# Optimization experiments

Hardware: AMD Instinct MI355X
Metric: run time of the kernel (lower is better)

## Reference

```python
import jax, jax.numpy as jnp
import numpy as np

B, L, D, N, R = 8, 64, 1024, 128, 64  # batch, seq(=channels), dim(=dim_inner), d_state, dt_rank


def setup_inputs() -> dict:
    key = jax.random.key(0)
    ks = jax.random.split(key, 8)
    sc = lambda k, sh, f: jax.random.normal(k, sh, jnp.float32) * f
    return {
        "x": sc(ks[0], (B, L, D), 1.0),
        "proj_w": sc(ks[1], (D, D), D ** -0.5),
        "proj_b": jnp.zeros((D,), jnp.float32),
        "conv_w": sc(ks[2], (L, L, 3), (L * 3) ** -0.5),  # (out_ch, in_ch, k)
        "conv_b": jnp.zeros((L,), jnp.float32),
        "dbc_w": sc(ks[3], (R + 2 * N, D), D ** -0.5),
        "dt_w": sc(ks[4], (D, R), R ** -0.5),
        "dt_b": sc(ks[5], (D,), 0.02),
        "A_log": jnp.log(jnp.broadcast_to(jnp.arange(1, N + 1, dtype=jnp.float32), (D, N))),
        "Dp": jnp.ones((D,), jnp.float32),
    }


def _ssm(x, dbc_w, dt_w, dt_b, A_log, Dp):
    # x: (B, L, ED) with ED == D
    A = -jnp.exp(A_log)                          # (ED, N)
    dbc = x @ dbc_w.T                            # (B, L, R + 2N)
    delta, Bm, Cm = jnp.split(dbc, [R, R + N], axis=-1)
    delta = jax.nn.softplus(delta @ dt_w.T + dt_b)            # (B, L, ED)
    dA = jnp.exp(delta[..., None] * A)                        # (B, L, ED, N)
    dBx = delta[..., None] * Bm[:, :, None, :] * x[..., None]  # (B, L, ED, N)

    def comb(c1, c2):
        a1, b1 = c1
        a2, b2 = c2
        return a1 * a2, a2 * b1 + b2

    _, hs = jax.lax.associative_scan(comb, (dA, dBx), axis=1)  # (B, L, ED, N)
    y = jnp.einsum("blen,bln->ble", hs, Cm)
    return y + Dp * x


def reference(x, proj_w, proj_b, conv_w, conv_b, dbc_w, dt_w, dt_b, A_log, Dp):
    skip = x
    xp = x @ proj_w.T + proj_b          # shared proj; x_one == x_two pre-activation
    x_two = jax.nn.silu(xp)
    # Conv1d treats seq axis (len L) as channels, convolving over the feature axis.
    x_one = jax.lax.conv_general_dilated(
        xp, conv_w, window_strides=(1,), padding=[(1, 1)],
        dimension_numbers=("NCH", "OIH", "NCH"),
    ) + conv_b[None, :, None]
    x_one = jax.nn.silu(x_one)
    x_one = _ssm(x_one, dbc_w, dt_w, dt_b, A_log, Dp)
    out = x_one * x_two + skip
    return out @ proj_w.T + proj_b
```

## Files before the change

kernel.cpp:

```cpp
#include <hip/hip_runtime.h>
#include <math.h>

#define B_ 8
#define L_ 64
#define D_ 1024
#define N_ 128
#define R_ 64

typedef unsigned short u16;
typedef __bf16 bf16x8 __attribute__((ext_vector_type(8)));
typedef u16 u16x8 __attribute__((ext_vector_type(8)));
typedef float floatx4 __attribute__((ext_vector_type(4)));

__device__ __forceinline__ float silu_f(float x) { return x / (1.f + __expf(-x)); }
__device__ __forceinline__ float softplus_f(float x) {
    return fmaxf(x, 0.f) + log1pf(__expf(-fabsf(x)));
}

__launch_bounds__(256)
__global__ void prep_bf16(const float* __restrict__ pw,
                          const float* __restrict__ dbcw,
                          const float* __restrict__ xin,
                          __bf16* __restrict__ pw_b,
                          __bf16* __restrict__ dbcw_b,
                          __bf16* __restrict__ x_b)
{
    int gid = blockIdx.x * 256 + threadIdx.x;
    const float* src; __bf16* dst; int off;
    if (gid < 131072)       { src = pw;   dst = pw_b;   off = gid * 8; }
    else if (gid < 172032)  { src = dbcw; dst = dbcw_b; off = (gid - 131072) * 8; }
    else if (gid < 237568)  { src = xin;  dst = x_b;    off = (gid - 172032) * 8; }
    else return;
    float4 f0 = *reinterpret_cast<const float4*>(src + off);
    float4 f1 = *reinterpret_cast<const float4*>(src + off + 4);
    bf16x8 v;
    v[0] = (__bf16)f0.x; v[1] = (__bf16)f0.y; v[2] = (__bf16)f0.z; v[3] = (__bf16)f0.w;
    v[4] = (__bf16)f1.x; v[5] = (__bf16)f1.y; v[6] = (__bf16)f1.z; v[7] = (__bf16)f1.w;
    *reinterpret_cast<bf16x8*>(dst + off) = v;
}

template <int ACT, int OUTF32>
__launch_bounds__(256)
__global__ void gemm_mfma(const u16* __restrict__ A, int lda,
                          const u16* __restrict__ W, int ldw,
                          const float* __restrict__ bias,
                          void* __restrict__ Cp, __bf16* __restrict__ C2,
                          int ldc, int K)
{
    __shared__ u16 As[32 * 64];
    __shared__ u16 Bs[64 * 64];
    const int tid = threadIdx.x;
    const int l   = tid & 63;
    const int w   = tid >> 6;
    const int wm  = w >> 1, wn = w & 1;
    const int m0  = blockIdx.y * 32;
    const int n0  = blockIdx.x * 64;

    const int ar = tid >> 3, ac = tid & 7;

    u16x8 sa, sb0, sb1;
    auto issue_loads = [&](int k0) {
        sa  = *reinterpret_cast<const u16x8*>(A + (size_t)(m0 + ar) * lda + k0 + ac * 8);
        sb0 = *reinterpret_cast<const u16x8*>(W + (size_t)(n0 + ar) * ldw + k0 + ac * 8);
        sb1 = *reinterpret_cast<const u16x8*>(W + (size_t)(n0 + 32 + ar) * ldw + k0 + ac * 8);
    };
    auto stage = [&]() {
        *reinterpret_cast<u16x8*>(&As[ar * 64 + ((ac ^ (ar & 7)) * 8)]) = sa;
        *reinterpret_cast<u16x8*>(&Bs[ar * 64 + ((ac ^ (ar & 7)) * 8)]) = sb0;
        const int r2 = 32 + ar;
        *reinterpret_cast<u16x8*>(&Bs[r2 * 64 + ((ac ^ (r2 & 7)) * 8)]) = sb1;
    };

    floatx4 acc[2] = {(floatx4)0.f, (floatx4)0.f};

    issue_loads(0);
    stage();
    __syncthreads();
    const int NT = K / 64;
    for (int t = 0; t < NT; ++t) {
        if (t + 1 < NT) issue_loads((t + 1) * 64);
        #pragma unroll
        for (int s = 0; s < 2; ++s) {
            const int ra = wm * 16 + (l & 15);
            const int ca = (s * 4 + (l >> 4)) ^ (ra & 7);
            bf16x8 a = *reinterpret_cast<const bf16x8*>(&As[ra * 64 + ca * 8]);
            #pragma unroll
            for (int nf = 0; nf < 2; ++nf) {
                const int rb = wn * 32 + nf * 16 + (l & 15);
                const int cb = (s * 4 + (l >> 4)) ^ (rb & 7);
                bf16x8 b = *reinterpret_cast<const bf16x8*>(&Bs[rb * 64 + cb * 8]);
                acc[nf] = __builtin_amdgcn_mfma_f32_16x16x32_bf16(a, b, acc[nf], 0, 0, 0);
            }
        }
        __syncthreads();
        if (t + 1 < NT) { stage(); __syncthreads(); }
    }

    #pragma unroll
    for (int nf = 0; nf < 2; ++nf) {
        const int n = n0 + wn * 32 + nf * 16 + (l & 15);
        const float bj = bias ? bias[n] : 0.f;
        #pragma unroll
        for (int r = 0; r < 4; ++r) {
            const int m = m0 + wm * 16 + (l >> 4) * 4 + r;
            float c = acc[nf][r] + bj;
            if (ACT == 2) c = softplus_f(c);
            const size_t idx = (size_t)m * ldc + n;
            if (OUTF32) ((float*)Cp)[idx] = c;
            else        ((__bf16*)Cp)[idx] = (__bf16)c;
            if (ACT == 1) C2[idx] = (__bf16)silu_f(c);
        }
    }
}

__launch_bounds__(256)
__global__ void conv_silu(const __bf16* __restrict__ xp,
                          const float* __restrict__ conv_w,
                          const float* __restrict__ conv_b,
                          __bf16* __restrict__ x_one)
{
    __shared__ float ws[192][65];
    __shared__ float xs[64][34];
    const int tid = threadIdx.x;
    const int b = blockIdx.y;
    const int d0 = blockIdx.x * 32;

    for (int idx = tid; idx < 64 * 64 * 3; idx += 256) {
        int lo = idx / 192, r = idx % 192;
        ws[r][lo] = conv_w[idx];
    }
    for (int idx = tid; idx < 64 * 34; idx += 256) {
        int li = idx / 34, dd = idx % 34;
        int g = d0 - 1 + dd;
        xs[li][dd] = (g >= 0 && g < D_) ? (float)xp[((size_t)b * L_ + li) * D_ + g] : 0.f;
    }
    __syncthreads();

    const int lo = tid >> 2;
    const int dbase = (tid & 3) * 8;
    float acc[8] = {};
    #pragma unroll 4
    for (int li = 0; li < 64; ++li) {
        float w0 = ws[li * 3 + 0][lo];
        float w1 = ws[li * 3 + 1][lo];
        float w2 = ws[li * 3 + 2][lo];
        float xv[10];
        #pragma unroll
        for (int j = 0; j < 10; ++j) xv[j] = xs[li][dbase + j];
        #pragma unroll
        for (int i = 0; i < 8; ++i)
            acc[i] = fmaf(w0, xv[i], fmaf(w1, xv[i + 1], fmaf(w2, xv[i + 2], acc[i])));
    }
    float bb = conv_b[lo];
    bf16x8 v;
    #pragma unroll
    for (int i = 0; i < 8; ++i) v[i] = (__bf16)silu_f(acc[i] + bb);
    *reinterpret_cast<bf16x8*>(&x_one[((size_t)b * L_ + lo) * D_ + d0 + dbase]) = v;
}

__launch_bounds__(256)
__global__ void ssm_scan(const __bf16* __restrict__ dbc,
                         const float* __restrict__ dt_w,
                         const float* __restrict__ dt_b,
                         const __bf16* __restrict__ xo_in,
                         const __bf16* __restrict__ xt_in,
                         const float* __restrict__ skip,
                         const float* __restrict__ A_log,
                         const float* __restrict__ Dp,
                         __bf16* __restrict__ out_mid)
{
    __shared__ u16 bcs[64][320];
    __shared__ float dtw_s[4][64];
    __shared__ float2 dlx[4][64];
    __shared__ float pt[4][16][65];
    const int tid = threadIdx.x;
    const int w = tid >> 6, ln = tid & 63;
    const int b = blockIdx.y;
    const int d = blockIdx.x * 4 + w;

    {
        const u16* src = (const u16*)dbc + (size_t)b * L_ * 320;
        #pragma unroll
        for (int i = tid; i < 2560; i += 256) {
            int lr = i / 40, c = i % 40;
            *reinterpret_cast<u16x8*>(&bcs[lr][c * 8]) =
                *reinterpret_cast<const u16x8*>(src + lr * 320 + c * 8);
        }
    }
    dtw_s[w][ln] = dt_w[(size_t)d * 64 + ln];
    const float xo_own = (float)xo_in[((size_t)b * L_ + ln) * D_ + d];
    const float a0 = -__expf(A_log[(size_t)d * N_ + ln]);
    const float a1 = -__expf(A_log[(size_t)d * N_ + 64 + ln]);
    const float dtb = dt_b[d];
    __syncthreads();

    float accd = dtb;
    #pragma unroll
    for (int k = 0; k < 64; ++k) {
        int kk = (k + ln) & 63;
        accd = fmaf((float)*reinterpret_cast<const __bf16*>(&bcs[ln][kk]),
                    dtw_s[w][kk], accd);
    }
    const float dl_own = softplus_f(accd);
    dlx[w][ln] = make_float2(dl_own, xo_own);
    __syncthreads();

    float h0 = 0.f, h1 = 0.f;
    float ych[4];
    const int rr = ln & 15, qq = ln >> 4;

    #pragma unroll
    for (int cch = 0; cch < 4; ++cch) {
        #pragma unroll
        for (int r = 0; r < 16; ++r) {
            const int l = cch * 16 + r;
            float2 dd = dlx[w][l];
            float dx = dd.x * dd.y;
            float B0 = (float)*reinterpret_cast<const __bf16*>(&bcs[l][64 + ln]);
            float B1 = (float)*reinterpret_cast<const __bf16*>(&bcs[l][128 + ln]);
            float C0 = (float)*reinterpret_cast<const __bf16*>(&bcs[l][192 + ln]);
            float C1 = (float)*reinterpret_cast<const __bf16*>(&bcs[l][256 + ln]);
            h0 = fmaf(__expf(dd.x * a0), h0, dx * B0);
            h1 = fmaf(__expf(dd.x * a1), h1, dx * B1);
            pt[w][r][ln] = fmaf(h0, C0, h1 * C1);
        }
        float sum = 0.f;
        #pragma unroll
        for (int j = 0; j < 4; ++j) {
            float4 v = *reinterpret_cast<const float4*>(&pt[w][rr][qq * 16 + j * 4]);
            sum += (v.x + v.y) + (v.z + v.w);
        }
        sum += __shfl_xor(sum, 16, 64);
        sum += __shfl_xor(sum, 32, 64);
        ych[cch] = sum;
    }

    float ysel = (qq == 0) ? ych[0] : (qq == 1) ? ych[1] : (qq == 2) ? ych[2] : ych[3];
    size_t idx = ((size_t)b * L_ + ln) * D_ + d;
    float y = ysel + Dp[d] * xo_own;
    out_mid[idx] = (__bf16)(y * (float)xt_in[idx] + skip[idx]);
}

extern "C" void kernel_launch(void* const* d_in, const int* in_sizes, int n_in,
                              void* d_out, int out_size, void* d_ws, size_t ws_size,
                              hipStream_t stream)
{
    const float* x      = (const float*)d_in[0];
    const float* proj_w = (const float*)d_in[1];
    const float* proj_b = (const float*)d_in[2];
    const float* conv_w = (const float*)d_in[3];
    const float* conv_b = (const float*)d_in[4];
    const float* dbc_w  = (const float*)d_in[5];
    const float* dt_w   = (const float*)d_in[6];
    const float* dt_b   = (const float*)d_in[7];
    const float* A_log  = (const float*)d_in[8];
    const float* Dp     = (const float*)d_in[9];
    float* out = (float*)d_out;

    __bf16* base    = (__bf16*)d_ws;
    __bf16* xp_b    = base;
    __bf16* xtwo_b  = xp_b + 524288;
    __bf16* xone_b  = xtwo_b + 524288;
    __bf16* dbc_b   = xone_b + 524288;
    __bf16* omid_b  = dbc_b + 163840;
    __bf16* pw_b    = omid_b + 524288;
    __bf16* dbcw_b  = pw_b + 1048576;
    __bf16* x_b     = dbcw_b + 327680;

    prep_bf16<<<928, 256, 0, stream>>>(proj_w, dbc_w, x, pw_b, dbcw_b, x_b);
    gemm_mfma<1, 0><<<dim3(16, 16), 256, 0, stream>>>(
        (const u16*)x_b, D_, (const u16*)pw_b, D_, proj_b, xp_b, xtwo_b, D_, D_);
    conv_silu<<<dim3(32, B_), 256, 0, stream>>>(xp_b, conv_w, conv_b, xone_b);
    gemm_mfma<0, 0><<<dim3(5, 16), 256, 0, stream>>>(
        (const u16*)xone_b, D_, (const u16*)dbcw_b, D_, nullptr, dbc_b, nullptr, 320, D_);
    ssm_scan<<<dim3(256, B_), 256, 0, stream>>>(
        dbc_b, dt_w, dt_b, xone_b, xtwo_b, x, A_log, Dp, omid_b);
    gemm_mfma<0, 1><<<dim3(16, 16), 256, 0, stream>>>(
        (const u16*)omid_b, D_, (const u16*)pw_b, D_, proj_b, out, nullptr, D_, D_);
}
```

Before: 163.1 us.

## Double-buffer GEMM smem, shrink tiles, transpose B/C output for vectorized scan reads

Result: faster. 156.7 us (-3.9%).

```diff
diff --git a/kernel.cpp b/kernel.cpp
--- a/kernel.cpp
+++ b/kernel.cpp
@@ -39,76 +39,101 @@
     *reinterpret_cast<bf16x8*>(dst + off) = v;
 }
 
-template <int ACT, int OUTF32>
-__launch_bounds__(256)
+template <int BM, int BN, int WM, int WN, int ACT, int OUTF32, int SPLIT>
+__launch_bounds__(WM * WN * 64)
 __global__ void gemm_mfma(const u16* __restrict__ A, int lda,
                           const u16* __restrict__ W, int ldw,
                           const float* __restrict__ bias,
                           void* __restrict__ Cp, __bf16* __restrict__ C2,
                           int ldc, int K)
 {
-    __shared__ u16 As[32 * 64];
-    __shared__ u16 Bs[64 * 64];
+    constexpr int NTHR = WM * WN * 64;
+    constexpr int NREP = BN / WN / 16;
+    constexpr int NA = BM * 8 / NTHR;
+    constexpr int NB = BN * 8 / NTHR;
+    __shared__ u16 As[2][BM * 64];
+    __shared__ u16 Bs[2][BN * 64];
     const int tid = threadIdx.x;
     const int l   = tid & 63;
     const int w   = tid >> 6;
-    const int wm  = w >> 1, wn = w & 1;
-    const int m0  = blockIdx.y * 32;
-    const int n0  = blockIdx.x * 64;
-
-    const int ar = tid >> 3, ac = tid & 7;
-
-    u16x8 sa, sb0, sb1;
+    const int wm  = w / WN, wn = w % WN;
+    const int m0  = blockIdx.y * BM;
+    const int n0  = blockIdx.x * BN;
+
+    u16x8 sa[NA], sb[NB];
     auto issue_loads = [&](int k0) {
-        sa  = *reinterpret_cast<const u16x8*>(A + (size_t)(m0 + ar) * lda + k0 + ac * 8);
-        sb0 = *reinterpret_cast<const u16x8*>(W + (size_t)(n0 + ar) * ldw + k0 + ac * 8);
-        sb1 = *reinterpret_cast<const u16x8*>(W + (size_t)(n0 + 32 + ar) * ldw + k0 + ac * 8);
+        #pragma unroll
+        for (int i = 0; i < NA; ++i) {
+            int idx = tid + i * NTHR, r = idx >> 3, c = idx & 7;
+            sa[i] = *reinterpret_cast<const u16x8*>(A + (size_t)(m0 + r) * lda + k0 + c * 8);
+        }
+        #pragma unroll
+        for (int i = 0; i < NB; ++i) {
+            int idx = tid + i * NTHR, r = idx >> 3, c = idx & 7;
+            sb[i] = *reinterpret_cast<const u16x8*>(W + (size_t)(n0 + r) * ldw + k0 + c * 8);
+        }
     };
-    auto stage = [&]() {
-        *reinterpret_cast<u16x8*>(&As[ar * 64 + ((ac ^ (ar & 7)) * 8)]) = sa;
-        *reinterpret_cast<u16x8*>(&Bs[ar * 64 + ((ac ^ (ar & 7)) * 8)]) = sb0;
-        const int r2 = 32 + ar;
-        *reinterpret_cast<u16x8*>(&Bs[r2 * 64 + ((ac ^ (r2 & 7)) * 8)]) = sb1;
+    auto stage = [&](int bb) {
+        #pragma unroll
+        for (int i = 0; i < NA; ++i) {
+            int idx = tid + i * NTHR, r = idx >> 3, c = idx & 7;
+            *reinterpret_cast<u16x8*>(&As[bb][r * 64 + ((c ^ (r & 7)) * 8)]) = sa[i];
+        }
+        #pragma unroll
+        for (int i = 0; i < NB; ++i) {
+            int idx = tid + i * NTHR, r = idx >> 3, c = idx & 7;
+            *reinterpret_cast<u16x8*>(&Bs[bb][r * 64 + ((c ^ (r & 7)) * 8)]) = sb[i];
+        }
     };
 
-    floatx4 acc[2] = {(floatx4)0.f, (floatx4)0.f};
+    floatx4 acc[NREP];
+    #pragma unroll
+    for (int i = 0; i < NREP; ++i) acc[i] = (floatx4)0.f;
 
     issue_loads(0);
-    stage();
+    stage(0);
     __syncthreads();
     const int NT = K / 64;
     for (int t = 0; t < NT; ++t) {
         if (t + 1 < NT) issue_loads((t + 1) * 64);
+        const int bb = t & 1;
         #pragma unroll
         for (int s = 0; s < 2; ++s) {
             const int ra = wm * 16 + (l & 15);
             const int ca = (s * 4 + (l >> 4)) ^ (ra & 7);
-            bf16x8 a = *reinterpret_cast<const bf16x8*>(&As[ra * 64 + ca * 8]);
+            bf16x8 a = *reinterpret_cast<const bf16x8*>(&As[bb][ra * 64 + ca * 8]);
             #pragma unroll
-            for (int nf = 0; nf < 2; ++nf) {
-                const int rb = wn * 32 + nf * 16 + (l & 15);
+            for (int nf = 0; nf < NREP; ++nf) {
+                const int rb = wn * (BN / WN) + nf * 16 + (l & 15);
                 const int cb = (s * 4 + (l >> 4)) ^ (rb & 7);
-                bf16x8 b = *reinterpret_cast<const bf16x8*>(&Bs[rb * 64 + cb * 8]);
+                bf16x8 b = *reinterpret_cast<const bf16x8*>(&Bs[bb][rb * 64 + cb * 8]);
                 acc[nf] = __builtin_amdgcn_mfma_f32_16x16x32_bf16(a, b, acc[nf], 0, 0, 0);
             }
         }
-        __syncthreads();
-        if (t + 1 < NT) { stage(); __syncthreads(); }
-    }
-
-    #pragma unroll
-    for (int nf = 0; nf < 2; ++nf) {
-        const int n = n0 + wn * 32 + nf * 16 + (l & 15);
+        if (t + 1 < NT) { stage((t + 1) & 1); __syncthreads(); }
+    }
+
+    #pragma unroll
+    for (int nf = 0; nf < NREP; ++nf) {
+        const int n = n0 + wn * (BN / WN) + nf * 16 + (l & 15);
         const float bj = bias ? bias[n] : 0.f;
         #pragma unroll
         for (int r = 0; r < 4; ++r) {
             const int m = m0 + wm * 16 + (l >> 4) * 4 + r;
             float c = acc[nf][r] + bj;
             if (ACT == 2) c = softplus_f(c);
-            const size_t idx = (size_t)m * ldc + n;
-            if (OUTF32) ((float*)Cp)[idx] = c;
-            else        ((__bf16*)Cp)[idx] = (__bf16)c;
-            if (ACT == 1) C2[idx] = (__bf16)silu_f(c);
+            if (SPLIT) {
+                if (n0 < 64) ((__bf16*)Cp)[(size_t)m * 64 + n] = (__bf16)c;
+                else {
+                    const int bb2 = m >> 6, ll = m & 63;
+                    C2[((size_t)bb2 * 256 + (n - 64)) * 64 + ll] = (__bf16)c;
+                }
+            } else {
+                const size_t idx = (size_t)m * ldc + n;
+                if (OUTF32) ((float*)Cp)[idx] = c;
+                else        ((__bf16*)Cp)[idx] = (__bf16)c;
+                if (ACT == 1) C2[idx] = (__bf16)silu_f(c);
+            }
         }
     }
 }
@@ -159,7 +184,8 @@
 }
 
 __launch_bounds__(256)
-__global__ void ssm_scan(const __bf16* __restrict__ dbc,
+__global__ void ssm_scan(const __bf16* __restrict__ dR,
+                         const __bf16* __restrict__ bct,
                          const float* __restrict__ dt_w,
                          const float* __restrict__ dt_b,
                          const __bf16* __restrict__ xo_in,
@@ -169,22 +195,30 @@
                          const float* __restrict__ Dp,
                          __bf16* __restrict__ out_mid)
 {
-    __shared__ u16 bcs[64][320];
+    __shared__ u16 bcts[256 * 66];
+    __shared__ u16 dRs[64 * 66];
     __shared__ float dtw_s[4][64];
     __shared__ float2 dlx[4][64];
-    __shared__ float pt[4][16][65];
+    __shared__ float pt[4][8][68];
     const int tid = threadIdx.x;
     const int w = tid >> 6, ln = tid & 63;
     const int b = blockIdx.y;
     const int d = blockIdx.x * 4 + w;
 
     {
-        const u16* src = (const u16*)dbc + (size_t)b * L_ * 320;
-        #pragma unroll
-        for (int i = tid; i < 2560; i += 256) {
-            int lr = i / 40, c = i % 40;
-            *reinterpret_cast<u16x8*>(&bcs[lr][c * 8]) =
-                *reinterpret_cast<const u16x8*>(src + lr * 320 + c * 8);
+        const u16* src = (const u16*)bct + (size_t)b * 256 * 64;
+        #pragma unroll
+        for (int i = tid; i < 2048; i += 256) {
+            int n = i >> 3, c = i & 7;
+            *reinterpret_cast<u16x8*>(&bcts[n * 66 + c * 8]) =
+                *reinterpret_cast<const u16x8*>(src + n * 64 + c * 8);
+        }
+        const u16* srcd = (const u16*)dR + (size_t)b * 64 * 64;
+        #pragma unroll
+        for (int i = tid; i < 512; i += 256) {
+            int r = i >> 3, c = i & 7;
+            *reinterpret_cast<u16x8*>(&dRs[r * 66 + c * 8]) =
+                *reinterpret_cast<const u16x8*>(srcd + r * 64 + c * 8);
         }
     }
     dtw_s[w][ln] = dt_w[(size_t)d * 64 + ln];
@@ -198,46 +232,45 @@
     #pragma unroll
     for (int k = 0; k < 64; ++k) {
         int kk = (k + ln) & 63;
-        accd = fmaf((float)*reinterpret_cast<const __bf16*>(&bcs[ln][kk]),
+        accd = fmaf((float)*reinterpret_cast<const __bf16*>(&dRs[ln * 66 + kk]),
                     dtw_s[w][kk], accd);
     }
     const float dl_own = softplus_f(accd);
     dlx[w][ln] = make_float2(dl_own, xo_own);
     __syncthreads();
 
-    float h0 = 0.f, h1 = 0.f;
-    float ych[4];
-    const int rr = ln & 15, qq = ln >> 4;
-
-    #pragma unroll
-    for (int cch = 0; cch < 4; ++cch) {
-        #pragma unroll
-        for (int r = 0; r < 16; ++r) {
-            const int l = cch * 16 + r;
+    float h0 = 0.f, h1 = 0.f, y_own = 0.f;
+    const int rr = ln & 7, qs = ln >> 3;
+
+    #pragma unroll
+    for (int cc = 0; cc < 8; ++cc) {
+        bf16x8 B0r = *reinterpret_cast<const bf16x8*>(&bcts[(      ln) * 66 + cc * 8]);
+        bf16x8 B1r = *reinterpret_cast<const bf16x8*>(&bcts[( 64 + ln) * 66 + cc * 8]);
+        bf16x8 C0r = *reinterpret_cast<const bf16x8*>(&bcts[(128 + ln) * 66 + cc * 8]);
+        bf16x8 C1r = *reinterpret_cast<const bf16x8*>(&bcts[(192 + ln) * 66 + cc * 8]);
+        #pragma unroll
+        for (int r = 0; r < 8; ++r) {
+            const int l = cc * 8 + r;
             float2 dd = dlx[w][l];
             float dx = dd.x * dd.y;
-            float B0 = (float)*reinterpret_cast<const __bf16*>(&bcs[l][64 + ln]);
-            float B1 = (float)*reinterpret_cast<const __bf16*>(&bcs[l][128 + ln]);
-            float C0 = (float)*reinterpret_cast<const __bf16*>(&bcs[l][192 + ln]);
-            float C1 = (float)*reinterpret_cast<const __bf16*>(&bcs[l][256 + ln]);
-            h0 = fmaf(__expf(dd.x * a0), h0, dx * B0);
-            h1 = fmaf(__expf(dd.x * a1), h1, dx * B1);
-            pt[w][r][ln] = fmaf(h0, C0, h1 * C1);
+            h0 = fmaf(__expf(dd.x * a0), h0, dx * (float)B0r[r]);
+            h1 = fmaf(__expf(dd.x * a1), h1, dx * (float)B1r[r]);
+            pt[w][r][ln] = fmaf(h0, (float)C0r[r], h1 * (float)C1r[r]);
         }
         float sum = 0.f;
         #pragma unroll
-        for (int j = 0; j < 4; ++j) {
-            float4 v = *reinterpret_cast<const float4*>(&pt[w][rr][qq * 16 + j * 4]);
+        for (int j = 0; j < 2; ++j) {
+            float4 v = *reinterpret_cast<const float4*>(&pt[w][rr][qs * 8 + j * 4]);
             sum += (v.x + v.y) + (v.z + v.w);
         }
+        sum += __shfl_xor(sum, 8, 64);
         sum += __shfl_xor(sum, 16, 64);
         sum += __shfl_xor(sum, 32, 64);
-        ych[cch] = sum;
-    }
-
-    float ysel = (qq == 0) ? ych[0] : (qq == 1) ? ych[1] : (qq == 2) ? ych[2] : ych[3];
+        if ((ln >> 3) == cc) y_own = sum;
+    }
+
     size_t idx = ((size_t)b * L_ + ln) * D_ + d;
-    float y = ysel + Dp[d] * xo_own;
+    float y = y_own + Dp[d] * xo_own;
     out_mid[idx] = (__bf16)(y * (float)xt_in[idx] + skip[idx]);
 }
 
@@ -261,20 +294,21 @@
     __bf16* xp_b    = base;
     __bf16* xtwo_b  = xp_b + 524288;
     __bf16* xone_b  = xtwo_b + 524288;
-    __bf16* dbc_b   = xone_b + 524288;
-    __bf16* omid_b  = dbc_b + 163840;
+    __bf16* dR_b    = xone_b + 524288;
+    __bf16* bct_b   = dR_b + 32768;
+    __bf16* omid_b  = bct_b + 131072;
     __bf16* pw_b    = omid_b + 524288;
     __bf16* dbcw_b  = pw_b + 1048576;
     __bf16* x_b     = dbcw_b + 327680;
 
     prep_bf16<<<928, 256, 0, stream>>>(proj_w, dbc_w, x, pw_b, dbcw_b, x_b);
-    gemm_mfma<1, 0><<<dim3(16, 16), 256, 0, stream>>>(
+    gemm_mfma<32, 32, 2, 2, 1, 0, 0><<<dim3(32, 16), 256, 0, stream>>>(
         (const u16*)x_b, D_, (const u16*)pw_b, D_, proj_b, xp_b, xtwo_b, D_, D_);
     conv_silu<<<dim3(32, B_), 256, 0, stream>>>(xp_b, conv_w, conv_b, xone_b);
-    gemm_mfma<0, 0><<<dim3(5, 16), 256, 0, stream>>>(
-        (const u16*)xone_b, D_, (const u16*)dbcw_b, D_, nullptr, dbc_b, nullptr, 320, D_);
+    gemm_mfma<16, 32, 1, 2, 0, 0, 1><<<dim3(10, 32), 128, 0, stream>>>(
+        (const u16*)xone_b, D_, (const u16*)dbcw_b, D_, nullptr, dR_b, bct_b, 320, D_);
     ssm_scan<<<dim3(256, B_), 256, 0, stream>>>(
-        dbc_b, dt_w, dt_b, xone_b, xtwo_b, x, A_log, Dp, omid_b);
-    gemm_mfma<0, 1><<<dim3(16, 16), 256, 0, stream>>>(
+        dR_b, bct_b, dt_w, dt_b, xone_b, xtwo_b, x, A_log, Dp, omid_b);
+    gemm_mfma<32, 32, 2, 2, 0, 1, 0><<<dim3(32, 16), 256, 0, stream>>>(
         (const u16*)omid_b, D_, (const u16*)pw_b, D_, proj_b, out, nullptr, D_, D_);
 }
```
